# Performance work log

Hardware: AMD Instinct MI355X
Metric: run time of the kernel (lower is better)

Reference implementation:

```python
import jax, jax.numpy as jnp
import numpy as np

N, E, G = 50000, 500000, 64
DIN, D, OUT, L = 64, 128, 10, 3


def setup_inputs() -> dict:
    key = jax.random.key(0)
    ks = iter(jax.random.split(key, 32))

    def nrm(shape, scale=0.05):
        return jax.random.normal(next(ks), shape, dtype=jnp.float32) * scale

    x = jax.random.normal(next(ks), (N, DIN), dtype=jnp.float32)
    edge_index = jax.random.randint(next(ks), (2, E), 0, N)
    batch = jnp.sort(jax.random.randint(next(ks), (N,), 0, G))
    return {
        "x": x,
        "edge_index": edge_index,
        "batch": batch,
        "num_graphs": G,
        # GIN encoder (gnn_node): input proj + L GIN layers (MLP: D->2D->D)
        "enc_in_W": nrm((DIN, D)), "enc_in_b": nrm((D,)),
        "enc_W1": nrm((L, D, 2 * D)), "enc_b1": nrm((L, 2 * D)),
        "enc_W2": nrm((L, 2 * D, D)), "enc_b2": nrm((L, D)),
        # edge attention MLP: Linear(2D, 4D) -> ReLU -> Linear(4D, 1)
        "att_W1": nrm((2 * D, 4 * D)), "att_b1": nrm((4 * D,)),
        "att_W2": nrm((4 * D, 1)), "att_b2": nrm((1,)),
        # classifier GNN on raw x (c_in='raw'), edge-weight-masked GIN
        "clf_in_W": nrm((DIN, D)), "clf_in_b": nrm((D,)),
        "clf_W1": nrm((L, D, 2 * D)), "clf_b1": nrm((L, 2 * D)),
        "clf_W2": nrm((L, 2 * D, D)), "clf_b2": nrm((L, D)),
        # prediction head after mean pooling
        "head_W": nrm((D, OUT)), "head_b": nrm((OUT,)),
    }


def reference(x, edge_index, batch, num_graphs,
              enc_in_W, enc_in_b, enc_W1, enc_b1, enc_W2, enc_b2,
              att_W1, att_b1, att_W2, att_b2,
              clf_in_W, clf_in_b, clf_W1, clf_b1, clf_W2, clf_b2,
              head_W, head_b):
    row, col = edge_index[0], edge_index[1]
    n = x.shape[0]

    def gin_layer(h, W1, b1, W2, b2, ew=None):
        msg = h[col]                         # gather [E, D]
        if ew is not None:
            msg = msg * ew[:, None]          # masked message passing
        agg = jax.ops.segment_sum(msg, row, num_segments=n)  # scatter-add [N, D]
        z = agg + h                          # (1 + eps) * h with eps = 0
        return jax.nn.relu(z @ W1 + b1) @ W2 + b2

    # ---- gnn_encoder: unweighted GIN over full graph ----
    h = jax.nn.relu(x @ enc_in_W + enc_in_b)
    nl = enc_W1.shape[0]
    for l in range(nl):
        h = gin_layer(h, enc_W1[l], enc_b1[l], enc_W2[l], enc_b2[l])
        if l < nl - 1:
            h = jax.nn.relu(h)

    # ---- edge attention MLP on [h_row, h_col] ----
    edge_rep = jnp.concatenate([h[row], h[col]], axis=-1)  # [E, 2D]
    logit = (jax.nn.relu(edge_rep @ att_W1 + att_b1) @ att_W2 + att_b2).reshape(-1)
    att = jax.nn.sigmoid(logit)  # concrete_sample, eval mode (deterministic)

    # ---- classifier GNN on raw x with edge-weight masks (set_masks) ----
    hc = jax.nn.relu(x @ clf_in_W + clf_in_b)
    for l in range(nl):
        hc = gin_layer(hc, clf_W1[l], clf_b1[l], clf_W2[l], clf_b2[l], ew=att)
        if l < nl - 1:
            hc = jax.nn.relu(hc)

    # ---- mean pooling per graph + linear head ----
    sums = jax.ops.segment_sum(hc, batch, num_segments=num_graphs)
    cnt = jax.ops.segment_sum(jnp.ones((n, 1), hc.dtype), batch, num_segments=num_graphs)
    pooled = sums / jnp.maximum(cnt, 1.0)
    return pooled @ head_W + head_b  # causal_pred [G, OUT]
```

## Files before the change

### kernel.cpp

```cpp
#include <hip/hip_runtime.h>
#include <hip/hip_bf16.h>
#include <cstddef>

#define kN 50000
#define kNP 50048
#define kE 500000
#define kG 64
#define kDIN 64
#define kD 128
#define kH 256
#define kA4 512
#define kOUT 10
#define PCHUNK 200
#define SBLK 196

typedef __attribute__((ext_vector_type(8))) short bfrag_t;
typedef __attribute__((ext_vector_type(4))) float f32x4;
typedef __attribute__((ext_vector_type(2))) float f32x2;
union FragCast { uint4 u; bfrag_t f; };

__device__ __attribute__((aligned(16))) __hip_bfloat16 g_h [(size_t)kNP * kD];
__device__ __attribute__((aligned(16))) __hip_bfloat16 g_hc[(size_t)kNP * kD];
__device__ __attribute__((aligned(16))) __hip_bfloat16 g_z [(size_t)kNP * kD];
__device__ __attribute__((aligned(16))) unsigned char  g_h8 [(size_t)kNP * kD];
__device__ __attribute__((aligned(16))) unsigned char  g_hc8[(size_t)kNP * kD];
__device__ __attribute__((aligned(16))) __hip_bfloat16 g_A [(size_t)kNP * kA4];
__device__ __attribute__((aligned(16))) unsigned char  g_Bf8[(size_t)kNP * kA4];
__device__ __attribute__((aligned(16))) __hip_bfloat16 g_pk[1056 * 512];
__device__ float g_atts[kE];
__device__ int   g_rowptr[kN + 1];
__device__ int   g_cnt[kN];
__device__ int   g_tmp[SBLK * 256];
__device__ int   g_bsum[256];
__device__ int   g_cols[kE];
__device__ float g_pool[kG * kD];
__device__ float g_gcnt[kG];

__device__ inline float bflo(unsigned u) { union { unsigned i; float f; } c; c.i = u << 16; return c.f; }
__device__ inline float bfhi(unsigned u) { union { unsigned i; float f; } c; c.i = u & 0xffff0000u; return c.f; }
__device__ inline __hip_bfloat16* bsel(int s) { return s == 0 ? g_h : (s == 1 ? g_hc : g_z); }

__device__ inline uint2 bf8pack(uint4 v) {
    float f[8];
    f[0] = bflo(v.x); f[1] = bfhi(v.x); f[2] = bflo(v.y); f[3] = bfhi(v.y);
    f[4] = bflo(v.z); f[5] = bfhi(v.z); f[6] = bflo(v.w); f[7] = bfhi(v.w);
    int w0 = __builtin_amdgcn_cvt_pk_fp8_f32(f[0], f[1], 0, false);
    w0 = __builtin_amdgcn_cvt_pk_fp8_f32(f[2], f[3], w0, true);
    int w1 = __builtin_amdgcn_cvt_pk_fp8_f32(f[4], f[5], 0, false);
    w1 = __builtin_amdgcn_cvt_pk_fp8_f32(f[6], f[7], w1, true);
    uint2 o; o.x = (unsigned)w0; o.y = (unsigned)w1;
    return o;
}

struct SrcPtrs { const float* p[16]; };

__global__ __launch_bounds__(64) void prepack_kernel(SrcPtrs sp) {
    const int fs[17] = {0,64,128,192,256,320,384,448,512,576,640,704,768,896,1024,1040,1056};
    const int Ns[16] = {256,256,256,128,128,128,256,256,256,128,128,128,512,512,128,128};
    int f = blockIdx.x;
    int m = 0;
    while (f >= fs[m + 1]) m++;
    const int fl = f - fs[m];
    const int N = Ns[m];
    const int n0 = fl % (N >> 4);
    const int k0 = fl / (N >> 4);
    const int lane = threadIdx.x;
    const int q = lane >> 4, c = lane & 15;
    const float* src = sp.p[m];
    __hip_bfloat16* dst = g_pk + (size_t)f * 512 + lane * 8;
    const int kb = k0 * 32 + q * 8;
    const int n = n0 * 16 + c;
#pragma unroll
    for (int j = 0; j < 8; j++)
        dst[j] = __float2bfloat16(src[(size_t)(kb + j) * N + n]);
}

#define PK_ENC_W1(l) ((size_t)(0   + (l) * 64) * 512)
#define PK_ENC_W2(l) ((size_t)(192 + (l) * 64) * 512)
#define PK_CLF_W1(l) ((size_t)(384 + (l) * 64) * 512)
#define PK_CLF_W2(l) ((size_t)(576 + (l) * 64) * 512)
#define PK_ATT_TOP   ((size_t)768 * 512)
#define PK_ATT_BOT   ((size_t)896 * 512)
#define PK_ENC_IN    ((size_t)1024 * 512)
#define PK_CLF_IN    ((size_t)1040 * 512)

__global__ __launch_bounds__(256) void zero_prep_kernel() {
    const int i = blockIdx.x * 256 + threadIdx.x;
    if (i < kN) g_cnt[i] = 0;
    if (i < kG * kD) g_pool[i] = 0.f;
    if (i < kG) g_gcnt[i] = 0.f;
}

__global__ __launch_bounds__(256) void hist_kernel(const int* __restrict__ row) {
    const int e = blockIdx.x * 256 + threadIdx.x;
    if (e < kE) atomicAdd(&g_cnt[row[e]], 1);
}

__global__ __launch_bounds__(256) void scan1_kernel() {
    __shared__ int sh[256];
    const int t = threadIdx.x;
    const int i = blockIdx.x * 256 + t;
    const int c = (i < kN) ? g_cnt[i] : 0;
    sh[t] = c;
    __syncthreads();
    int v = c;
    for (int off = 1; off < 256; off <<= 1) {
        int add = (t >= off) ? sh[t - off] : 0;
        __syncthreads();
        v += add;
        sh[t] = v;
        __syncthreads();
    }
    g_tmp[i] = v - c;
    if (t == 255) g_bsum[blockIdx.x] = v;
}

__global__ __launch_bounds__(256) void scan2_kernel() {
    __shared__ int sh[256];
    const int t = threadIdx.x;
    const int c = (t < SBLK) ? g_bsum[t] : 0;
    sh[t] = c;
    __syncthreads();
    int v = c;
    for (int off = 1; off < 256; off <<= 1) {
        int add = (t >= off) ? sh[t - off] : 0;
        __syncthreads();
        v += add;
        sh[t] = v;
        __syncthreads();
    }
    if (t < SBLK) g_bsum[t] = v - c;
}

__global__ __launch_bounds__(256) void scan3_kernel() {
    const int i = blockIdx.x * 256 + threadIdx.x;
    const int v = g_tmp[i] + g_bsum[blockIdx.x];
    if (i <= kN) g_rowptr[i] = v;
    if (i < kN) g_cnt[i] = v;
}

__global__ __launch_bounds__(256) void scatter_kernel(
    const int* __restrict__ row, const int* __restrict__ col) {
    const int e = blockIdx.x * 256 + threadIdx.x;
    if (e >= kE) return;
    const int r = row[e];
    const int pos = atomicAdd(&g_cnt[r], 1);
    g_cols[pos] = col[e];
}

__global__ __launch_bounds__(256) void input_proj_mfma(
    const float* __restrict__ x,
    const float* __restrict__ eb, const float* __restrict__ cb) {
    __shared__ __hip_bfloat16 xs[64][72];
    __shared__ __hip_bfloat16 ob[64][264];
    const int t = threadIdx.x, lane = t & 63, w = t >> 6;
    const int node0 = blockIdx.x * 64;
#pragma unroll
    for (int it = 0; it < 4; it++) {
        int idx = t + it * 256;
        int r = idx >> 4, c = idx & 15;
        float4 v = make_float4(0.f, 0.f, 0.f, 0.f);
        if (node0 + r < kN) v = ((const float4*)x)[(size_t)(node0 + r) * 16 + c];
        union { uint2 u; __hip_bfloat16 h[4]; } o;
        o.h[0] = __float2bfloat16(v.x); o.h[1] = __float2bfloat16(v.y);
        o.h[2] = __float2bfloat16(v.z); o.h[3] = __float2bfloat16(v.w);
        *(uint2*)(&xs[r][c * 4]) = o.u;
    }
    __syncthreads();
    const int q = lane >> 4, cidx = lane & 15;
    f32x4 acc[4][4] = {};
    const uint4* pk = (const uint4*)(g_pk + (w >= 2 ? PK_CLF_IN : PK_ENC_IN));
#pragma unroll
    for (int k0 = 0; k0 < 2; k0++) {
        FragCast a[4], b[4];
#pragma unroll
        for (int mt = 0; mt < 4; mt++)
            a[mt].u = *(const uint4*)(&xs[mt * 16 + cidx][k0 * 32 + q * 8]);
#pragma unroll
        for (int nt = 0; nt < 4; nt++)
            b[nt].u = pk[(size_t)(k0 * 8 + (w & 1) * 4 + nt) * 64 + lane];
#pragma unroll
        for (int mt = 0; mt < 4; mt++)
#pragma unroll
            for (int nt = 0; nt < 4; nt++)
                acc[mt][nt] = __builtin_amdgcn_mfma_f32_16x16x32_bf16(
                    a[mt].f, b[nt].f, acc[mt][nt], 0, 0, 0);
    }
    const float* bp = (w >= 2) ? cb : eb;
#pragma unroll
    for (int nt = 0; nt < 4; nt++) {
        const int mcol = (w & 1) * 64 + nt * 16 + cidx;
        const float bv = bp[mcol];
#pragma unroll
        for (int mt = 0; mt < 4; mt++)
#pragma unroll
            for (int r = 0; r < 4; r++)
                ob[mt * 16 + q * 4 + r][w * 64 + nt * 16 + cidx] =
                    __float2bfloat16(fmaxf(acc[mt][nt][r] + bv, 0.f));
    }
    __syncthreads();
#pragma unroll
    for (int it = 0; it < 8; it++) {
        int idx = t + it * 256;
        int r = idx >> 5, c = idx & 31;
        uint4 v = *(const uint4*)(&ob[r][c * 8]);
        uint2 v8 = bf8pack(v);
        if (c < 16) {
            ((uint4*)(g_h  + (size_t)(node0 + r) * kD))[c] = v;
            ((uint2*)(g_h8 + (size_t)(node0 + r) * kD))[c] = v8;
        } else {
            ((uint4*)(g_hc  + (size_t)(node0 + r) * kD))[c - 16] = v;
            ((uint2*)(g_hc8 + (size_t)(node0 + r) * kD))[c - 16] = v8;
        }
    }
}

__device__ inline void f8acc(uint2 v, f32x2 wt, f32x2& c0, f32x2& c1, f32x2& c2, f32x2& c3) {
    c0 = c0 + __builtin_amdgcn_cvt_pk_f32_fp8(v.x, false) * wt;
    c1 = c1 + __builtin_amdgcn_cvt_pk_f32_fp8(v.x, true)  * wt;
    c2 = c2 + __builtin_amdgcn_cvt_pk_f32_fp8(v.y, false) * wt;
    c3 = c3 + __builtin_amdgcn_cvt_pk_f32_fp8(v.y, true)  * wt;
}
__device__ inline void f8sum(uint2 v, f32x2& c0, f32x2& c1, f32x2& c2, f32x2& c3) {
    c0 = c0 + __builtin_amdgcn_cvt_pk_f32_fp8(v.x, false);
    c1 = c1 + __builtin_amdgcn_cvt_pk_f32_fp8(v.x, true);
    c2 = c2 + __builtin_amdgcn_cvt_pk_f32_fp8(v.y, false);
    c3 = c3 + __builtin_amdgcn_cvt_pk_f32_fp8(v.y, true);
}

__global__ __launch_bounds__(256) void agg_csr_kernel(int src_sel, int use_att) {
    const int t = threadIdx.x;
    const int node = blockIdx.x * 16 + (t >> 4);
    const int li = t & 15;
    const uint4* __restrict__ src  = (const uint4*)bsel(src_sel);
    const uint2* __restrict__ src8 = (const uint2*)(src_sel == 0 ? g_h8 : g_hc8);
    f32x2 c0 = {0.f, 0.f}, c1 = {0.f, 0.f}, c2 = {0.f, 0.f}, c3 = {0.f, 0.f};
    if (node < kN) {
        const uint4 sv = src[(size_t)node * 16 + li];
        c0 = (f32x2){bflo(sv.x), bfhi(sv.x)};
        c1 = (f32x2){bflo(sv.y), bfhi(sv.y)};
        c2 = (f32x2){bflo(sv.z), bfhi(sv.z)};
        c3 = (f32x2){bflo(sv.w), bfhi(sv.w)};
        const int beg = g_rowptr[node], end = g_rowptr[node + 1];
        int j = beg;
        if (use_att) {
            for (; j + 4 <= end; j += 4) {
                const uint2 v0 = src8[(size_t)g_cols[j    ] * 16 + li];
                const uint2 v1 = src8[(size_t)g_cols[j + 1] * 16 + li];
                const uint2 v2 = src8[(size_t)g_cols[j + 2] * 16 + li];
                const uint2 v3 = src8[(size_t)g_cols[j + 3] * 16 + li];
                const float w0 = g_atts[j],     w1 = g_atts[j + 1];
                const float w2 = g_atts[j + 2], w3 = g_atts[j + 3];
                f8acc(v0, (f32x2){w0, w0}, c0, c1, c2, c3);
                f8acc(v1, (f32x2){w1, w1}, c0, c1, c2, c3);
                f8acc(v2, (f32x2){w2, w2}, c0, c1, c2, c3);
                f8acc(v3, (f32x2){w3, w3}, c0, c1, c2, c3);
            }
            for (; j < end; j++) {
                const uint2 v = src8[(size_t)g_cols[j] * 16 + li];
                const float wt = g_atts[j];
                f8acc(v, (f32x2){wt, wt}, c0, c1, c2, c3);
            }
        } else {
            for (; j + 4 <= end; j += 4) {
                const uint2 v0 = src8[(size_t)g_cols[j    ] * 16 + li];
                const uint2 v1 = src8[(size_t)g_cols[j + 1] * 16 + li];
                const uint2 v2 = src8[(size_t)g_cols[j + 2] * 16 + li];
                const uint2 v3 = src8[(size_t)g_cols[j + 3] * 16 + li];
                f8sum(v0, c0, c1, c2, c3);
                f8sum(v1, c0, c1, c2, c3);
                f8sum(v2, c0, c1, c2, c3);
                f8sum(v3, c0, c1, c2, c3);
            }
            for (; j < end; j++) {
                const uint2 v = src8[(size_t)g_cols[j] * 16 + li];
                f8sum(v, c0, c1, c2, c3);
            }
        }
    }
    union { uint4 u; __hip_bfloat16 h[8]; } o;
    o.h[0] = __float2bfloat16(c0.x); o.h[1] = __float2bfloat16(c0.y);
    o.h[2] = __float2bfloat16(c1.x); o.h[3] = __float2bfloat16(c1.y);
    o.h[4] = __float2bfloat16(c2.x); o.h[5] = __float2bfloat16(c2.y);
    o.h[6] = __float2bfloat16(c3.x); o.h[7] = __float2bfloat16(c3.y);
    ((uint4*)g_z)[(size_t)node * 16 + li] = o.u;
}

__global__ __launch_bounds__(256) void gin_mlp_mfma(
    int dst_sel, size_t pkW1off, size_t pkW2off,
    const float* __restrict__ b1, const float* __restrict__ b2, int relu_out) {
    __shared__ __hip_bfloat16 zs[64][136];
    __shared__ __hip_bfloat16 hid[64][264];
    const int t = threadIdx.x, lane = t & 63, w = t >> 6;
    const int node0 = blockIdx.x * 64;
    __hip_bfloat16* hp = bsel(dst_sel);
    unsigned char* mp = dst_sel == 0 ? g_h8 : g_hc8;

    {
        const uint4* src = (const uint4*)(g_z + (size_t)node0 * kD);
#pragma unroll
        for (int it = 0; it < 4; it++) {
            int idx = t + it * 256;
            int r = idx >> 4, c = idx & 15;
            *(uint4*)(&zs[r][c * 8]) = src[(size_t)r * 16 + c];
        }
    }
    __syncthreads();

    const int q = lane >> 4, cidx = lane & 15;

    f32x4 acc1[4][4] = {};
    const uint4* pk1 = (const uint4*)(g_pk + pkW1off);
    for (int k0 = 0; k0 < 4; k0++) {
        FragCast a[4], b[4];
#pragma unroll
        for (int mt = 0; mt < 4; mt++)
            a[mt].u = *(const uint4*)(&zs[mt * 16 + cidx][k0 * 32 + q * 8]);
#pragma unroll
        for (int nt = 0; nt < 4; nt++)
            b[nt].u = pk1[(size_t)(k0 * 16 + (w * 4 + nt)) * 64 + lane];
#pragma unroll
        for (int mt = 0; mt < 4; mt++)
#pragma unroll
            for (int nt = 0; nt < 4; nt++)
                acc1[mt][nt] = __builtin_amdgcn_mfma_f32_16x16x32_bf16(
                    a[mt].f, b[nt].f, acc1[mt][nt], 0, 0, 0);
    }
#pragma unroll
    for (int nt = 0; nt < 4; nt++) {
        const int col = w * 64 + nt * 16 + cidx;
        const float bv = b1[col];
#pragma unroll
        for (int mt = 0; mt < 4; mt++)
#pragma unroll
            for (int r = 0; r < 4; r++)
                hid[mt * 16 + q * 4 + r][col] =
                    __float2bfloat16(fmaxf(acc1[mt][nt][r] + bv, 0.f));
    }
    __syncthreads();

    f32x4 acc2[4][2] = {};
    const uint4* pk2 = (const uint4*)(g_pk + pkW2off);
    for (int k0 = 0; k0 < 8; k0++) {
        FragCast a[4], b[2];
#pragma unroll
        for (int mt = 0; mt < 4; mt++)
            a[mt].u = *(const uint4*)(&hid[mt * 16 + cidx][k0 * 32 + q * 8]);
#pragma unroll
        for (int nt = 0; nt < 2; nt++)
            b[nt].u = pk2[(size_t)(k0 * 8 + (w * 2 + nt)) * 64 + lane];
#pragma unroll
        for (int mt = 0; mt < 4; mt++)
#pragma unroll
            for (int nt = 0; nt < 2; nt++)
                acc2[mt][nt] = __builtin_amdgcn_mfma_f32_16x16x32_bf16(
                    a[mt].f, b[nt].f, acc2[mt][nt], 0, 0, 0);
    }
#pragma unroll
    for (int nt = 0; nt < 2; nt++) {
        const int col = w * 32 + nt * 16 + cidx;
        const float bv = b2[col];
#pragma unroll
        for (int mt = 0; mt < 4; mt++)
#pragma unroll
            for (int r = 0; r < 4; r++) {
                float v = acc2[mt][nt][r] + bv;
                if (relu_out) v = fmaxf(v, 0.f);
                zs[mt * 16 + q * 4 + r][col] = __float2bfloat16(v);
            }
    }
    __syncthreads();
    {
        uint4* dst = (uint4*)(hp + (size_t)node0 * kD);
        uint2* md  = (uint2*)(mp + (size_t)node0 * kD);
#pragma unroll
        for (int it = 0; it < 4; it++) {
            int idx = t + it * 256;
            int r = idx >> 4, c = idx & 15;
            uint4 v = *(const uint4*)(&zs[r][c * 8]);
            dst[(size_t)r * 16 + c] = v;
            md[(size_t)r * 16 + c] = bf8pack(v);
        }
    }
}

__global__ __launch_bounds__(256) void att_dense_mfma(const float* __restrict__ b1) {
    __shared__ __hip_bfloat16 zs[64][136];
    __shared__ __hip_bfloat16 ob[64][264];
    const int t = threadIdx.x, lane = t & 63, w = t >> 6;
    const int node0 = blockIdx.x * 64;
    const int mat = blockIdx.y >> 1, half = blockIdx.y & 1;
    const size_t pkoff = mat ? PK_ATT_BOT : PK_ATT_TOP;

    const uint4* src = (const uint4*)(g_h + (size_t)node0 * kD);
#pragma unroll
    for (int it = 0; it < 4; it++) {
        int idx = t + it * 256;
        int r = idx >> 4, c = idx & 15;
        *(uint4*)(&zs[r][c * 8]) = src[(size_t)r * 16 + c];
    }
    __syncthreads();

    const int q = lane >> 4, cidx = lane & 15;
    f32x4 acc[4][4] = {};
    const uint4* pk = (const uint4*)(g_pk + pkoff);
    for (int k0 = 0; k0 < 4; k0++) {
        FragCast a[4], b[4];
#pragma unroll
        for (int mt = 0; mt < 4; mt++)
            a[mt].u = *(const uint4*)(&zs[mt * 16 + cidx][k0 * 32 + q * 8]);
#pragma unroll
        for (int nt = 0; nt < 4; nt++)
            b[nt].u = pk[(size_t)(k0 * 32 + (half * 16 + w * 4 + nt)) * 64 + lane];
#pragma unroll
        for (int mt = 0; mt < 4; mt++)
#pragma unroll
            for (int nt = 0; nt < 4; nt++)
                acc[mt][nt] = __builtin_amdgcn_mfma_f32_16x16x32_bf16(
                    a[mt].f, b[nt].f, acc[mt][nt], 0, 0, 0);
    }
#pragma unroll
    for (int nt = 0; nt < 4; nt++) {
        const int lcol = w * 64 + nt * 16 + cidx;
        const float bv = (mat == 0) ? b1[half * 256 + lcol] : 0.f;
#pragma unroll
        for (int mt = 0; mt < 4; mt++)
#pragma unroll
            for (int r = 0; r < 4; r++)
                ob[mt * 16 + q * 4 + r][lcol] = __float2bfloat16(acc[mt][nt][r] + bv);
    }
    __syncthreads();
    if (mat == 0) {
        uint4* dst = (uint4*)(g_A + (size_t)node0 * kA4 + half * 256);
#pragma unroll
        for (int it = 0; it < 8; it++) {
            int idx = t + it * 256;
            int r = idx >> 5, c = idx & 31;
            dst[(size_t)r * 64 + c] = *(const uint4*)(&ob[r][c * 8]);
        }
    } else {
        uint2* dst = (uint2*)(g_Bf8 + (size_t)node0 * kA4 + half * 256);
#pragma unroll
        for (int it = 0; it < 8; it++) {
            int idx = t + it * 256;
            int r = idx >> 5, c = idx & 31;
            dst[(size_t)r * 64 + c] = bf8pack(*(const uint4*)(&ob[r][c * 8]));
        }
    }
}

__device__ inline float edge_dot16_f8(const f32x2* a2, const f32x2* w2, uint4 bu) {
    const f32x2 zero = {0.f, 0.f};
    f32x2 p = zero;
    const unsigned wd[4] = {bu.x, bu.y, bu.z, bu.w};
#pragma unroll
    for (int k = 0; k < 4; k++) {
        f32x2 b0 = __builtin_amdgcn_cvt_pk_f32_fp8(wd[k], false);
        f32x2 b1 = __builtin_amdgcn_cvt_pk_f32_fp8(wd[k], true);
        f32x2 t0 = __builtin_elementwise_max(a2[2 * k] + b0, zero);
        f32x2 t1 = __builtin_elementwise_max(a2[2 * k + 1] + b1, zero);
        p = p + t0 * w2[2 * k];
        p = p + t1 * w2[2 * k + 1];
    }
    return p.x + p.y;
}

__global__ __launch_bounds__(256) void att_edge_csr(
    const float* __restrict__ W2, const float* __restrict__ b2) {
    const int node = blockIdx.x * 4 + (threadIdx.x >> 6);
    const int lane = threadIdx.x & 63;
    const int sub = lane >> 5;
    const int li  = lane & 31;
    const int m0 = li * 16;
    const uint4 au0 = *(const uint4*)(g_A + (size_t)node * kA4 + m0);
    const uint4 au1 = *(const uint4*)(g_A + (size_t)node * kA4 + m0 + 8);
    f32x2 a2[8];
    a2[0] = (f32x2){bflo(au0.x), bfhi(au0.x)};
    a2[1] = (f32x2){bflo(au0.y), bfhi(au0.y)};
    a2[2] = (f32x2){bflo(au0.z), bfhi(au0.z)};
    a2[3] = (f32x2){bflo(au0.w), bfhi(au0.w)};
    a2[4] = (f32x2){bflo(au1.x), bfhi(au1.x)};
    a2[5] = (f32x2){bflo(au1.y), bfhi(au1.y)};
    a2[6] = (f32x2){bflo(au1.z), bfhi(au1.z)};
    a2[7] = (f32x2){bflo(au1.w), bfhi(au1.w)};
    f32x2 w2[8];
#pragma unroll
    for (int k = 0; k < 8; k++) {
        const float2 wk = *(const float2*)(W2 + m0 + 2 * k);
        w2[k] = (f32x2){wk.x, wk.y};
    }
    const float bb = b2[0];
    const int beg = g_rowptr[node], end = g_rowptr[node + 1];

    int j = beg;
    for (; j + 8 <= end; j += 8) {
        const int c0 = g_cols[j + sub];
        const int c1 = g_cols[j + 2 + sub];
        const int c2 = g_cols[j + 4 + sub];
        const int c3 = g_cols[j + 6 + sub];
        const uint4 b0 = *(const uint4*)(g_Bf8 + (size_t)c0 * kA4 + m0);
        const uint4 b1 = *(const uint4*)(g_Bf8 + (size_t)c1 * kA4 + m0);
        const uint4 b2v = *(const uint4*)(g_Bf8 + (size_t)c2 * kA4 + m0);
        const uint4 b3 = *(const uint4*)(g_Bf8 + (size_t)c3 * kA4 + m0);
        float s0 = edge_dot16_f8(a2, w2, b0);
        float s1 = edge_dot16_f8(a2, w2, b1);
        float s2 = edge_dot16_f8(a2, w2, b2v);
        float s3 = edge_dot16_f8(a2, w2, b3);
        for (int off = 16; off > 0; off >>= 1) {
            s0 += __shfl_down(s0, off);
            s1 += __shfl_down(s1, off);
            s2 += __shfl_down(s2, off);
            s3 += __shfl_down(s3, off);
        }
        if (li == 0) {
            g_atts[j + sub]     = 1.f / (1.f + __expf(-(s0 + bb)));
            g_atts[j + 2 + sub] = 1.f / (1.f + __expf(-(s1 + bb)));
            g_atts[j + 4 + sub] = 1.f / (1.f + __expf(-(s2 + bb)));
            g_atts[j + 6 + sub] = 1.f / (1.f + __expf(-(s3 + bb)));
        }
    }
    for (; j + 4 <= end; j += 4) {
        const int c0 = g_cols[j + sub];
        const int c1 = g_cols[j + 2 + sub];
        const uint4 b0 = *(const uint4*)(g_Bf8 + (size_t)c0 * kA4 + m0);
        const uint4 b1 = *(const uint4*)(g_Bf8 + (size_t)c1 * kA4 + m0);
        float s0 = edge_dot16_f8(a2, w2, b0);
        float s1 = edge_dot16_f8(a2, w2, b1);
        for (int off = 16; off > 0; off >>= 1) {
            s0 += __shfl_down(s0, off);
            s1 += __shfl_down(s1, off);
        }
        if (li == 0) {
            g_atts[j + sub]     = 1.f / (1.f + __expf(-(s0 + bb)));
            g_atts[j + 2 + sub] = 1.f / (1.f + __expf(-(s1 + bb)));
        }
    }
    for (; j < end; j += 2) {
        const int je = j + sub;
        const int jc = (je < end) ? je : (end - 1);
        const int c = g_cols[jc];
        const uint4 b0 = *(const uint4*)(g_Bf8 + (size_t)c * kA4 + m0);
        float s = edge_dot16_f8(a2, w2, b0);
        for (int off = 16; off > 0; off >>= 1) s += __shfl_down(s, off);
        if (li == 0 && je < end)
            g_atts[je] = 1.f / (1.f + __expf(-(s + bb)));
    }
}

__global__ __launch_bounds__(64) void pool_kernel(const int* __restrict__ batch) {
    const int t = threadIdx.x;
    int n = blockIdx.x * PCHUNK;
    const int nend = n + PCHUNK;
    const unsigned* __restrict__ hc = (const unsigned*)g_hc;
    int gcur = batch[n];
    float a0 = 0.f, a1 = 0.f, cv = 0.f;
    for (; n < nend; n++) {
        const int g = batch[n];
        if (g != gcur) {
            atomicAdd(&g_pool[gcur * kD + 2 * t], a0);
            atomicAdd(&g_pool[gcur * kD + 2 * t + 1], a1);
            if (t == 0) atomicAdd(&g_gcnt[gcur], cv);
            a0 = a1 = cv = 0.f; gcur = g;
        }
        unsigned v = hc[(size_t)n * 64 + t];
        a0 += bflo(v); a1 += bfhi(v);
        cv += 1.f;
    }
    atomicAdd(&g_pool[gcur * kD + 2 * t], a0);
    atomicAdd(&g_pool[gcur * kD + 2 * t + 1], a1);
    if (t == 0) atomicAdd(&g_gcnt[gcur], cv);
}

__global__ __launch_bounds__(640) void head_kernel(
    const float* __restrict__ hW, const float* __restrict__ hb,
    float* __restrict__ out) {
    const int t = threadIdx.x;
    const int g = t / kOUT, o = t - g * kOUT;
    const float c = fmaxf(g_gcnt[g], 1.f);
    const float inv = 1.f / c;
    float acc = hb[o];
    for (int k = 0; k < kD; k++)
        acc = fmaf(g_pool[g * kD + k] * inv, hW[k * kOUT + o], acc);
    out[(size_t)g * kOUT + o] = acc;
}

extern "C" void kernel_launch(void* const* d_in, const int* in_sizes, int n_in,
                              void* d_out, int out_size, void* d_ws, size_t ws_size,
                              hipStream_t stream) {
    const float* x        = (const float*)d_in[0];
    const int*   ei       = (const int*)d_in[1];
    const int*   row      = ei;
    const int*   col      = ei + kE;
    const int*   batch    = (const int*)d_in[2];
    const float* enc_in_W = (const float*)d_in[4];
    const float* enc_in_b = (const float*)d_in[5];
    const float* enc_W1   = (const float*)d_in[6];
    const float* enc_b1   = (const float*)d_in[7];
    const float* enc_W2   = (const float*)d_in[8];
    const float* enc_b2   = (const float*)d_in[9];
    const float* att_W1   = (const float*)d_in[10];
    const float* att_b1   = (const float*)d_in[11];
    const float* att_W2   = (const float*)d_in[12];
    const float* att_b2   = (const float*)d_in[13];
    const float* clf_in_W = (const float*)d_in[14];
    const float* clf_in_b = (const float*)d_in[15];
    const float* clf_W1   = (const float*)d_in[16];
    const float* clf_b1   = (const float*)d_in[17];
    const float* clf_W2   = (const float*)d_in[18];
    const float* clf_b2   = (const float*)d_in[19];
    const float* head_W   = (const float*)d_in[20];
    const float* head_b   = (const float*)d_in[21];
    float* out = (float*)d_out;

    const dim3 blk(256);
    const int eblocks = (kE + 255) / 256;

    SrcPtrs sp;
    for (int l = 0; l < 3; l++) {
        sp.p[0 + l] = enc_W1 + (size_t)l * kD * kH;
        sp.p[3 + l] = enc_W2 + (size_t)l * kH * kD;
        sp.p[6 + l] = clf_W1 + (size_t)l * kD * kH;
        sp.p[9 + l] = clf_W2 + (size_t)l * kH * kD;
    }
    sp.p[12] = att_W1;
    sp.p[13] = att_W1 + (size_t)kD * kA4;
    sp.p[14] = enc_in_W;
    sp.p[15] = clf_in_W;
    prepack_kernel<<<1056, dim3(64), 0, stream>>>(sp);

    zero_prep_kernel<<<(kN + 255) / 256, blk, 0, stream>>>();
    hist_kernel<<<eblocks, blk, 0, stream>>>(row);
    scan1_kernel<<<SBLK, blk, 0, stream>>>();
    scan2_kernel<<<1, blk, 0, stream>>>();
    scan3_kernel<<<SBLK, blk, 0, stream>>>();
    scatter_kernel<<<eblocks, blk, 0, stream>>>(row, col);

    input_proj_mfma<<<kNP / 64, blk, 0, stream>>>(x, enc_in_b, clf_in_b);

    for (int l = 0; l < 3; l++) {
        agg_csr_kernel<<<kNP / 16, blk, 0, stream>>>(0, 0);
        gin_mlp_mfma<<<kNP / 64, blk, 0, stream>>>(
            0, PK_ENC_W1(l), PK_ENC_W2(l),
            enc_b1 + (size_t)l * kH, enc_b2 + (size_t)l * kD, (l < 2) ? 1 : 0);
    }

    att_dense_mfma<<<dim3(kNP / 64, 4), blk, 0, stream>>>(att_b1);
    att_edge_csr<<<kN / 4, blk, 0, stream>>>(att_W2, att_b2);

    for (int l = 0; l < 3; l++) {
        agg_csr_kernel<<<kNP / 16, blk, 0, stream>>>(1, 1);
        gin_mlp_mfma<<<kNP / 64, blk, 0, stream>>>(
            1, PK_CLF_W1(l), PK_CLF_W2(l),
            clf_b1 + (size_t)l * kH, clf_b2 + (size_t)l * kD, (l < 2) ? 1 : 0);
    }

    pool_kernel<<<kN / PCHUNK, dim3(64), 0, stream>>>(batch);
    head_kernel<<<1, dim3(kG * kOUT), 0, stream>>>(head_W, head_b, out);
}
```

Before: 574.4 us.

## Fuse edge attention computation with first classifier aggregation layer

```diff
diff --git a/kernel.cpp b/kernel.cpp
--- a/kernel.cpp
+++ b/kernel.cpp
@@ -226,6 +226,16 @@
     c1 = c1 + __builtin_amdgcn_cvt_pk_f32_fp8(v.x, true);
     c2 = c2 + __builtin_amdgcn_cvt_pk_f32_fp8(v.y, false);
     c3 = c3 + __builtin_amdgcn_cvt_pk_f32_fp8(v.y, true);
+}
+__device__ inline void f8acc4(uint4 v, f32x2 wt, f32x2* c) {
+    c[0] = c[0] + __builtin_amdgcn_cvt_pk_f32_fp8(v.x, false) * wt;
+    c[1] = c[1] + __builtin_amdgcn_cvt_pk_f32_fp8(v.x, true)  * wt;
+    c[2] = c[2] + __builtin_amdgcn_cvt_pk_f32_fp8(v.y, false) * wt;
+    c[3] = c[3] + __builtin_amdgcn_cvt_pk_f32_fp8(v.y, true)  * wt;
+    c[4] = c[4] + __builtin_amdgcn_cvt_pk_f32_fp8(v.z, false) * wt;
+    c[5] = c[5] + __builtin_amdgcn_cvt_pk_f32_fp8(v.z, true)  * wt;
+    c[6] = c[6] + __builtin_amdgcn_cvt_pk_f32_fp8(v.w, false) * wt;
+    c[7] = c[7] + __builtin_amdgcn_cvt_pk_f32_fp8(v.w, true)  * wt;
 }
 
 __global__ __launch_bounds__(256) void agg_csr_kernel(int src_sel, int use_att) {
@@ -465,7 +475,7 @@
     return p.x + p.y;
 }
 
-__global__ __launch_bounds__(256) void att_edge_csr(
+__global__ __launch_bounds__(256) void att_agg_fused(
     const float* __restrict__ W2, const float* __restrict__ b2) {
     const int node = blockIdx.x * 4 + (threadIdx.x >> 6);
     const int lane = threadIdx.x & 63;
@@ -483,67 +493,87 @@
     a2[5] = (f32x2){bflo(au1.y), bfhi(au1.y)};
     a2[6] = (f32x2){bflo(au1.z), bfhi(au1.z)};
     a2[7] = (f32x2){bflo(au1.w), bfhi(au1.w)};
-    f32x2 w2[8];
+    f32x2 w2r[8];
 #pragma unroll
     for (int k = 0; k < 8; k++) {
         const float2 wk = *(const float2*)(W2 + m0 + 2 * k);
-        w2[k] = (f32x2){wk.x, wk.y};
+        w2r[k] = (f32x2){wk.x, wk.y};
     }
     const float bb = b2[0];
+
+    f32x2 acc[8] = {};
+    if (sub == 0 && li < 8) {
+        const uint4 s0 = ((const uint4*)g_hc)[(size_t)node * 16 + 2 * li];
+        const uint4 s1 = ((const uint4*)g_hc)[(size_t)node * 16 + 2 * li + 1];
+        acc[0] = (f32x2){bflo(s0.x), bfhi(s0.x)};
+        acc[1] = (f32x2){bflo(s0.y), bfhi(s0.y)};
+        acc[2] = (f32x2){bflo(s0.z), bfhi(s0.z)};
+        acc[3] = (f32x2){bflo(s0.w), bfhi(s0.w)};
+        acc[4] = (f32x2){bflo(s1.x), bfhi(s1.x)};
+        acc[5] = (f32x2){bflo(s1.y), bfhi(s1.y)};
+        acc[6] = (f32x2){bflo(s1.z), bfhi(s1.z)};
+        acc[7] = (f32x2){bflo(s1.w), bfhi(s1.w)};
+    }
     const int beg = g_rowptr[node], end = g_rowptr[node + 1];
 
     int j = beg;
-    for (; j + 8 <= end; j += 8) {
-        const int c0 = g_cols[j + sub];
-        const int c1 = g_cols[j + 2 + sub];
-        const int c2 = g_cols[j + 4 + sub];
-        const int c3 = g_cols[j + 6 + sub];
-        const uint4 b0 = *(const uint4*)(g_Bf8 + (size_t)c0 * kA4 + m0);
-        const uint4 b1 = *(const uint4*)(g_Bf8 + (size_t)c1 * kA4 + m0);
-        const uint4 b2v = *(const uint4*)(g_Bf8 + (size_t)c2 * kA4 + m0);
-        const uint4 b3 = *(const uint4*)(g_Bf8 + (size_t)c3 * kA4 + m0);
-        float s0 = edge_dot16_f8(a2, w2, b0);
-        float s1 = edge_dot16_f8(a2, w2, b1);
-        float s2 = edge_dot16_f8(a2, w2, b2v);
-        float s3 = edge_dot16_f8(a2, w2, b3);
-        for (int off = 16; off > 0; off >>= 1) {
-            s0 += __shfl_down(s0, off);
-            s1 += __shfl_down(s1, off);
-            s2 += __shfl_down(s2, off);
-            s3 += __shfl_down(s3, off);
-        }
-        if (li == 0) {
-            g_atts[j + sub]     = 1.f / (1.f + __expf(-(s0 + bb)));
-            g_atts[j + 2 + sub] = 1.f / (1.f + __expf(-(s1 + bb)));
-            g_atts[j + 4 + sub] = 1.f / (1.f + __expf(-(s2 + bb)));
-            g_atts[j + 6 + sub] = 1.f / (1.f + __expf(-(s3 + bb)));
-        }
-    }
     for (; j + 4 <= end; j += 4) {
         const int c0 = g_cols[j + sub];
         const int c1 = g_cols[j + 2 + sub];
         const uint4 b0 = *(const uint4*)(g_Bf8 + (size_t)c0 * kA4 + m0);
         const uint4 b1 = *(const uint4*)(g_Bf8 + (size_t)c1 * kA4 + m0);
-        float s0 = edge_dot16_f8(a2, w2, b0);
-        float s1 = edge_dot16_f8(a2, w2, b1);
+        float s0 = edge_dot16_f8(a2, w2r, b0);
+        float s1 = edge_dot16_f8(a2, w2r, b1);
         for (int off = 16; off > 0; off >>= 1) {
             s0 += __shfl_down(s0, off);
             s1 += __shfl_down(s1, off);
         }
+        const float att0 = 1.f / (1.f + __expf(-(__shfl(s0, sub * 32) + bb)));
+        const float att1 = 1.f / (1.f + __expf(-(__shfl(s1, sub * 32) + bb)));
         if (li == 0) {
-            g_atts[j + sub]     = 1.f / (1.f + __expf(-(s0 + bb)));
-            g_atts[j + 2 + sub] = 1.f / (1.f + __expf(-(s1 + bb)));
+            g_atts[j + sub]     = att0;
+            g_atts[j + 2 + sub] = att1;
+        }
+        if (li < 8) {
+            const uint4 m0v = ((const uint4*)g_hc8)[(size_t)c0 * 8 + li];
+            const uint4 m1v = ((const uint4*)g_hc8)[(size_t)c1 * 8 + li];
+            f8acc4(m0v, (f32x2){att0, att0}, acc);
+            f8acc4(m1v, (f32x2){att1, att1}, acc);
         }
     }
     for (; j < end; j += 2) {
         const int je = j + sub;
-        const int jc = (je < end) ? je : (end - 1);
-        const int c = g_cols[jc];
+        const bool ok = je < end;
+        const int c = g_cols[ok ? je : end - 1];
         const uint4 b0 = *(const uint4*)(g_Bf8 + (size_t)c * kA4 + m0);
-        float s = edge_dot16_f8(a2, w2, b0);
+        float s = edge_dot16_f8(a2, w2r, b0);
         for (int off = 16; off > 0; off >>= 1) s += __shfl_down(s, off);
-        if (li == 0 && je < end)
-            g_atts[je] = 1.f / (1.f + __expf(-(s + bb)));
+        const float att = 1.f / (1.f + __expf(-(__shfl(s, sub * 32) + bb)));
+        if (ok) {
+            if (li == 0) g_atts[je] = att;
+            if (li < 8) {
+                const uint4 mv = ((const uint4*)g_hc8)[(size_t)c * 8 + li];
+                f8acc4(mv, (f32x2){att, att}, acc);
+            }
+        }
+    }
+#pragma unroll
+    for (int r = 0; r < 8; r++) {
+        acc[r].x += __shfl(acc[r].x, lane ^ 32);
+        acc[r].y += __shfl(acc[r].y, lane ^ 32);
+    }
+    if (sub == 0 && li < 8) {
+        union { uint4 u; __hip_bfloat16 h[8]; } o0, o1;
+        o0.h[0] = __float2bfloat16(acc[0].x); o0.h[1] = __float2bfloat16(acc[0].y);
+        o0.h[2] = __float2bfloat16(acc[1].x); o0.h[3] = __float2bfloat16(acc[1].y);
+        o0.h[4] = __float2bfloat16(acc[2].x); o0.h[5] = __float2bfloat16(acc[2].y);
+        o0.h[6] = __float2bfloat16(acc[3].x); o0.h[7] = __float2bfloat16(acc[3].y);
+        o1.h[0] = __float2bfloat16(acc[4].x); o1.h[1] = __float2bfloat16(acc[4].y);
+        o1.h[2] = __float2bfloat16(acc[5].x); o1.h[3] = __float2bfloat16(acc[5].y);
+        o1.h[4] = __float2bfloat16(acc[6].x); o1.h[5] = __float2bfloat16(acc[6].y);
+        o1.h[6] = __float2bfloat16(acc[7].x); o1.h[7] = __float2bfloat16(acc[7].y);
+        ((uint4*)g_z)[(size_t)node * 16 + 2 * li]     = o0.u;
+        ((uint4*)g_z)[(size_t)node * 16 + 2 * li + 1] = o1.u;
     }
 }
 
@@ -645,9 +675,11 @@
     }
 
     att_dense_mfma<<<dim3(kNP / 64, 4), blk, 0, stream>>>(att_b1);
-    att_edge_csr<<<kN / 4, blk, 0, stream>>>(att_W2, att_b2);
-
-    for (int l = 0; l < 3; l++) {
+    att_agg_fused<<<kN / 4, blk, 0, stream>>>(att_W2, att_b2);
+    gin_mlp_mfma<<<kNP / 64, blk, 0, stream>>>(
+        1, PK_CLF_W1(0), PK_CLF_W2(0), clf_b1, clf_b2, 1);
+
+    for (int l = 1; l < 3; l++) {
         agg_csr_kernel<<<kNP / 16, blk, 0, stream>>>(1, 1);
         gin_mlp_mfma<<<kNP / 64, blk, 0, stream>>>(
             1, PK_CLF_W1(l), PK_CLF_W2(l),
```

After: 596.6 us. 3.9% more time.
